# Performance work log

Measured on AMD Instinct MI355X. Metric: run time of the kernel, lower is better.

Reference implementation:

```python
import jax, jax.numpy as jnp
import numpy as np

SHAPES = ((100, 100), (50, 50), (25, 25))  # (H_l, W_l) per level
D, HEADS, HD, L, P = 256, 8, 32, 3, 4


def setup_inputs() -> dict:
    key = jax.random.key(0)
    ks = jax.random.split(key, 12)
    B = 2
    Nq = sum(h * w for h, w in SHAPES)  # 13125
    inp = {
        "query": jax.random.normal(ks[0], (B, Nq, D), jnp.float32),
        "reference_points": jax.random.uniform(ks[1], (B, Nq, L, 2), jnp.float32),
        "value0": jax.random.normal(ks[2], (B, SHAPES[0][0] * SHAPES[0][1], D), jnp.float32),
        "value1": jax.random.normal(ks[3], (B, SHAPES[1][0] * SHAPES[1][1], D), jnp.float32),
        "value2": jax.random.normal(ks[4], (B, SHAPES[2][0] * SHAPES[2][1], D), jnp.float32),
        "W_val": jax.random.normal(ks[5], (D, D), jnp.float32) * 0.05,
        "b_val": jnp.zeros((D,), jnp.float32),
        "W_off": jax.random.normal(ks[6], (D, HEADS * L * P * 2), jnp.float32) * 0.01,
        "b_off": jax.random.normal(ks[7], (HEADS * L * P * 2,), jnp.float32) * 2.0,
        "W_attn": jax.random.normal(ks[8], (D, HEADS * L * P), jnp.float32) * 0.02,
        "b_attn": jnp.zeros((HEADS * L * P,), jnp.float32),
        "W_out": jax.random.normal(ks[9], (D, D), jnp.float32) * 0.05,
        "b_out": jnp.zeros((D,), jnp.float32),
    }
    return inp


def _bilinear_sample(v, Hl, Wl, loc):
    """v: (B, heads, Hl*Wl, hd); loc: (B, Nq, heads, P, 2) normalized coords in [0,1].
    Matches torch F.grid_sample(mode='bilinear', padding_mode='zeros', align_corners=False)
    applied to grid = 2*loc - 1. Returns (B, Nq, heads, P, hd)."""
    B, heads, _, hd = v.shape
    Nq, Pn = loc.shape[1], loc.shape[3]
    # align_corners=False: pixel = ((g+1)*size - 1)/2 with g = 2*loc-1  ->  loc*size - 0.5
    x = loc[..., 0] * Wl - 0.5
    y = loc[..., 1] * Hl - 0.5
    x0 = jnp.floor(x)
    y0 = jnp.floor(y)
    wx1 = x - x0
    wy1 = y - y0
    out = jnp.zeros((B, Nq, heads, Pn, hd), v.dtype)
    for xi, wx in ((x0, 1.0 - wx1), (x0 + 1.0, wx1)):
        for yi, wy in ((y0, 1.0 - wy1), (y0 + 1.0, wy1)):
            inb = (xi >= 0) & (xi < Wl) & (yi >= 0) & (yi < Hl)
            idx = (jnp.clip(yi, 0, Hl - 1) * Wl + jnp.clip(xi, 0, Wl - 1)).astype(jnp.int32)
            idx_t = idx.transpose(0, 2, 1, 3).reshape(B, heads, Nq * Pn)  # (B,H,Nq*P)
            g = jnp.take_along_axis(v, idx_t[..., None], axis=2)  # (B,H,Nq*P,hd)
            g = g.reshape(B, heads, Nq, Pn, hd).transpose(0, 2, 1, 3, 4)
            w = (wx * wy * inb).astype(v.dtype)  # (B,Nq,heads,P)
            out = out + g * w[..., None]
    return out


def _forward(query, reference_points, values, W_val, b_val, W_off, b_off, W_attn, b_attn, W_out, b_out):
    B, Nq, _ = query.shape
    offs = (query @ W_off + b_off).reshape(B, Nq, HEADS, L, P, 2)
    attn = jax.nn.softmax((query @ W_attn + b_attn).reshape(B, Nq, HEADS, L * P), axis=-1)
    attn = attn.reshape(B, Nq, HEADS, L, P)
    out = jnp.zeros((B, Nq, HEADS, HD), query.dtype)
    for lvl, (Hl, Wl) in enumerate(SHAPES):
        # project values, split heads: (B, heads, H*W, hd)
        v = (values[lvl] @ W_val + b_val).reshape(B, Hl * Wl, HEADS, HD).transpose(0, 2, 1, 3)
        norm = jnp.array([Wl, Hl], query.dtype)
        loc = reference_points[:, :, lvl][:, :, None, None, :] + offs[:, :, :, lvl] / norm  # (B,Nq,heads,P,2)
        sampled = _bilinear_sample(v, Hl, Wl, loc)  # (B,Nq,heads,P,hd)
        out = out + jnp.einsum('bnhp,bnhpd->bnhd', attn[:, :, :, lvl], sampled)
    out = out.reshape(B, Nq, D)
    return out @ W_out + b_out  # dropout is identity at eval


def reference(query, reference_points, value0, value1, value2, W_val, b_val, W_off, b_off, W_attn, b_attn, W_out, b_out):
    return _forward(query, reference_points, (value0, value1, value2), W_val, b_val, W_off, b_off, W_attn, b_attn, W_out, b_out)
```

## Files before the change

kernel.cpp:

```cpp
#include <hip/hip_runtime.h>
#include <hip/hip_bf16.h>
#include <math.h>

#define BATCH 2
#define NQ    13125
#define MQ    26250
#define DM    256
#define NH    8
#define HDIM  32
#define NL    3
#define NP    4
#define NTOK  13125

typedef __attribute__((ext_vector_type(8))) short bf16x8;
typedef __attribute__((ext_vector_type(4))) float f32x4;
typedef __attribute__((ext_vector_type(2))) float f32x2;

__device__ __forceinline__ short f2bf(float f) {
    unsigned u = __float_as_uint(f);
    unsigned r = (u + 0x7FFFu + ((u >> 16) & 1u)) >> 16;
    return (short)r;
}
__device__ __forceinline__ float bf2f(unsigned short u) {
    return __uint_as_float((unsigned)u << 16);
}
__device__ __forceinline__ unsigned cvt_pk_bf16(float lo, float hi) {
    unsigned r;
    asm("v_cvt_pk_bf16_f32 %0, %1, %2" : "=v"(r) : "v"(lo), "v"(hi));
    return r;
}

__device__ __forceinline__ void gld_lds16(const short* g, short* l) {
    __builtin_amdgcn_global_load_lds(
        (const __attribute__((address_space(1))) unsigned int*)g,
        (__attribute__((address_space(3))) unsigned int*)l, 16, 0, 0);
}

__global__ __launch_bounds__(256) void wprep_kernel(const float* __restrict__ Wv,
                                                    const float* __restrict__ Wo,
                                                    const float* __restrict__ Wa,
                                                    const float* __restrict__ Wu,
                                                    short* __restrict__ Wt)
{
    const int bid = blockIdx.x;
    const int w  = bid >> 8;
    const int Ns[5]   = {256, 192, 96, 256, 96};
    const int Offs[5] = {0, 65536, 114688, 163840, 139264};
    const int N = Ns[w];
    const int flat = (bid & 255) * 256 + threadIdx.x;
    const int n = flat >> 8, k = flat & 255;
    if (n >= N) return;
    if (w == 4) { Wt[139264 + n * 256 + k] = 0; return; }
    const float* W = (w == 0) ? Wv : ((w == 1) ? Wo : ((w == 2) ? Wa : Wu));
    Wt[Offs[w] + n * 256 + k] = f2bf(W[k * N + n]);
}

__global__ __launch_bounds__(256) void gemm5_kernel(const float* __restrict__ query,
                                                    const float* __restrict__ v0,
                                                    const float* __restrict__ v1,
                                                    const float* __restrict__ v2,
                                                    const short* __restrict__ Wt_val,
                                                    const short* __restrict__ Wt_off,
                                                    const float* __restrict__ b_val,
                                                    const float* __restrict__ b_off,
                                                    const float* __restrict__ b_attn,
                                                    short* __restrict__ vws,
                                                    float* __restrict__ offs,
                                                    float* __restrict__ lgts)
{
    __shared__ short As[128 * 32];
    __shared__ short Bs[128 * 32];

    const int tid  = threadIdx.x;
    const int y    = blockIdx.y;
    const int m0   = blockIdx.x * 128;
    const bool isv = (y < 2);
    const short* Wt = isv ? Wt_val : Wt_off;
    const int n0 = isv ? y * 128 : (y - 2) * 128;

    const int r  = tid >> 1;
    const int h  = tid & 1;
    const int gm = m0 + r;
    const int gmc = (gm < MQ) ? gm : (MQ - 1);
    const float* Arow;
    if (isv) {
        const int b  = gmc / NTOK;
        const int rr = gmc % NTOK;
        if (rr < 10000)      Arow = v0 + (size_t)(b * 10000 + rr) * 256;
        else if (rr < 12500) Arow = v1 + (size_t)(b * 2500 + rr - 10000) * 256;
        else                 Arow = v2 + (size_t)(b * 625 + rr - 12500) * 256;
    } else {
        Arow = query + (size_t)gmc * 256;
    }
    const int pA0 = ((h * 2 + 0) ^ ((r >> 1) & 3)) << 3;
    const int pA1 = ((h * 2 + 1) ^ ((r >> 1) & 3)) << 3;
    short* lAr = As + r * 32;

    const int row0 = tid >> 2;
    const int row1 = row0 + 64;
    const int kqs  = (tid & 3) ^ ((row0 >> 1) & 3);
    const short* gB0 = Wt + (size_t)(n0 + row0) * 256 + kqs * 8;
    const short* gB1 = Wt + (size_t)(n0 + row1) * 256 + kqs * 8;
    short* lB0 = Bs + tid * 8;
    short* lB1 = Bs + (256 + tid) * 8;

    const int lane = tid & 63;
    const int wave = tid >> 6;
    const int wm   = (wave & 1) * 64;
    const int wn   = (wave >> 1) * 64;
    const int ml   = lane & 15;
    const int kq   = lane >> 4;

    f32x4 acc[4][4] = {};

    for (int k0 = 0; k0 < 256; k0 += 32) {
        gld_lds16(gB0 + k0, lB0);
        gld_lds16(gB1 + k0, lB1);

        const float4 a0 = *(const float4*)(Arow + k0 + h * 16 + 0);
        const float4 a1 = *(const float4*)(Arow + k0 + h * 16 + 4);
        const float4 a2 = *(const float4*)(Arow + k0 + h * 16 + 8);
        const float4 a3 = *(const float4*)(Arow + k0 + h * 16 + 12);
        union { bf16x8 v; unsigned u[4]; } t0, t1;
        t0.u[0] = cvt_pk_bf16(a0.x, a0.y); t0.u[1] = cvt_pk_bf16(a0.z, a0.w);
        t0.u[2] = cvt_pk_bf16(a1.x, a1.y); t0.u[3] = cvt_pk_bf16(a1.z, a1.w);
        t1.u[0] = cvt_pk_bf16(a2.x, a2.y); t1.u[1] = cvt_pk_bf16(a2.z, a2.w);
        t1.u[2] = cvt_pk_bf16(a3.x, a3.y); t1.u[3] = cvt_pk_bf16(a3.z, a3.w);
        *(bf16x8*)(lAr + pA0) = t0.v;
        *(bf16x8*)(lAr + pA1) = t1.v;

        __syncthreads();

        bf16x8 af[4], bfr[4];
#pragma unroll
        for (int ti = 0; ti < 4; ++ti) {
            const int rr = wm + ti * 16 + ml;
            af[ti] = *(const bf16x8*)&As[rr * 32 + ((kq ^ ((rr >> 1) & 3)) << 3)];
        }
#pragma unroll
        for (int tj = 0; tj < 4; ++tj) {
            const int rr = wn + tj * 16 + ml;
            bfr[tj] = *(const bf16x8*)&Bs[rr * 32 + ((kq ^ ((rr >> 1) & 3)) << 3)];
        }
#pragma unroll
        for (int ti = 0; ti < 4; ++ti)
#pragma unroll
            for (int tj = 0; tj < 4; ++tj)
                acc[ti][tj] = __builtin_amdgcn_mfma_f32_16x16x32_bf16(af[ti], bfr[tj], acc[ti][tj], 0, 0, 0);

        __syncthreads();
    }

#pragma unroll
    for (int tj = 0; tj < 4; ++tj) {
        const int gn = n0 + wn + tj * 16 + ml;
#pragma unroll
        for (int ti = 0; ti < 4; ++ti) {
#pragma unroll
            for (int rr = 0; rr < 4; ++rr) {
                const int gmo = m0 + wm + ti * 16 + kq * 4 + rr;
                if (gmo >= MQ) continue;
                const float v = acc[ti][tj][rr];
                if (isv) {
                    vws[(size_t)gmo * 256 + gn] = f2bf(v + b_val[gn]);
                } else {
                    if (gn < 192)      offs[(size_t)gmo * 192 + gn]        = v + b_off[gn];
                    else if (gn < 288) lgts[(size_t)gmo * 96 + (gn - 192)] = v + b_attn[gn - 192];
                }
            }
        }
    }
}

__device__ __forceinline__ void gemm_core128(const short* __restrict__ A,
                                             const short* __restrict__ Wt,
                                             int m0, int n0,
                                             f32x4 (&acc)[4][4],
                                             short* As, short* Bs)
{
    const int tid  = threadIdx.x;
    const int lane = tid & 63;
    const int wave = tid >> 6;
    const int wm   = (wave & 1) * 64;
    const int wn   = (wave >> 1) * 64;
    const int ml   = lane & 15;
    const int kq   = lane >> 4;

    const int row0 = tid >> 2;
    const int row1 = row0 + 64;
    const int kqs  = (tid & 3) ^ ((row0 >> 1) & 3);
    const short* gA0 = A  + (size_t)(m0 + row0) * 256 + kqs * 8;
    const short* gA1 = A  + (size_t)(m0 + row1) * 256 + kqs * 8;
    const short* gB0 = Wt + (size_t)(n0 + row0) * 256 + kqs * 8;
    const short* gB1 = Wt + (size_t)(n0 + row1) * 256 + kqs * 8;
    short* lA0 = As + tid * 8;
    short* lA1 = As + (256 + tid) * 8;
    short* lB0 = Bs + tid * 8;
    short* lB1 = Bs + (256 + tid) * 8;
    const bool a0ok = (m0 + row0) < MQ;
    const bool a1ok = (m0 + row1) < MQ;

    for (int k0 = 0; k0 < 256; k0 += 32) {
        if (a0ok) gld_lds16(gA0 + k0, lA0);
        if (a1ok) gld_lds16(gA1 + k0, lA1);
        gld_lds16(gB0 + k0, lB0);
        gld_lds16(gB1 + k0, lB1);
        __syncthreads();

        bf16x8 af[4], bfr[4];
#pragma unroll
        for (int ti = 0; ti < 4; ++ti) {
            const int r = wm + ti * 16 + ml;
            af[ti] = *(const bf16x8*)&As[r * 32 + ((kq ^ ((r >> 1) & 3)) << 3)];
        }
#pragma unroll
        for (int tj = 0; tj < 4; ++tj) {
            const int r = wn + tj * 16 + ml;
            bfr[tj] = *(const bf16x8*)&Bs[r * 32 + ((kq ^ ((r >> 1) & 3)) << 3)];
        }
#pragma unroll
        for (int ti = 0; ti < 4; ++ti)
#pragma unroll
            for (int tj = 0; tj < 4; ++tj)
                acc[ti][tj] = __builtin_amdgcn_mfma_f32_16x16x32_bf16(af[ti], bfr[tj], acc[ti][tj], 0, 0, 0);

        __syncthreads();
    }
}

__global__ __launch_bounds__(256) void ogemm_kernel(const short* __restrict__ A,
                                                    const short* __restrict__ Wt,
                                                    const float* __restrict__ bias,
                                                    float* __restrict__ C)
{
    __shared__ short As[128 * 32];
    __shared__ short Bs[128 * 32];
    const int m0 = blockIdx.y * 128;
    const int n0 = blockIdx.x * 128;

    f32x4 acc[4][4] = {};
    gemm_core128(A, Wt, m0, n0, acc, As, Bs);

    const int tid  = threadIdx.x;
    const int lane = tid & 63;
    const int wave = tid >> 6;
    const int wm   = (wave & 1) * 64;
    const int wn   = (wave >> 1) * 64;
    const int ml   = lane & 15;
    const int kq   = lane >> 4;

#pragma unroll
    for (int tj = 0; tj < 4; ++tj) {
        const int gn = n0 + wn + tj * 16 + ml;
#pragma unroll
        for (int ti = 0; ti < 4; ++ti) {
#pragma unroll
            for (int r = 0; r < 4; ++r) {
                const int gm = m0 + wm + ti * 16 + kq * 4 + r;
                if (gm >= MQ) continue;
                C[(size_t)gm * 256 + gn] = acc[ti][tj][r] + bias[gn];
            }
        }
    }
}

__device__ __forceinline__ void pk_acc(f32x2 (&acc)[4], uint4 u, float w) {
    f32x2 w2 = {w, w};
    unsigned ud[4] = {u.x, u.y, u.z, u.w};
#pragma unroll
    for (int d = 0; d < 4; ++d) {
        f32x2 v2;
        v2.x = __uint_as_float(ud[d] << 16);
        v2.y = __uint_as_float(ud[d] & 0xFFFF0000u);
        asm("v_pk_fma_f32 %0, %1, %2, %0" : "+v"(acc[d]) : "v"(v2), "v"(w2));
    }
}

__global__ __launch_bounds__(256) void sample_kernel(const short* __restrict__ vws,
                                                     const float* __restrict__ offs,
                                                     const float* __restrict__ logits,
                                                     const float* __restrict__ refp,
                                                     short* __restrict__ mid)
{
    const int q0  = blockIdx.x * 8;
    const int tid = threadIdx.x;

    __shared__ float  s_lg[8][96];
    __shared__ float  s_ref[8][6];
    __shared__ float  s_stat[8][NH][2];
    __shared__ float4 s_w[8][96];
    __shared__ int4   s_i[8][96];

    for (int idx = tid; idx < 768; idx += 256) {
        const int qq = idx / 96, s = idx % 96;
        const int q = q0 + qq;
        if (q < MQ) s_lg[qq][s] = logits[(size_t)q * 96 + s];
    }
    if (tid < 48) {
        const int qq = tid / 6, j = tid % 6;
        const int q = q0 + qq;
        if (q < MQ) s_ref[qq][j] = refp[(size_t)q * 6 + j];
    }
    __syncthreads();

    if (tid < 64) {
        const int qq = tid >> 3, h = tid & 7;
        if (q0 + qq < MQ) {
            float mx = -1e30f;
#pragma unroll
            for (int i = 0; i < 12; ++i) mx = fmaxf(mx, s_lg[qq][h * 12 + i]);
            float ssum = 0.f;
#pragma unroll
            for (int i = 0; i < 12; ++i) ssum += __expf(s_lg[qq][h * 12 + i] - mx);
            s_stat[qq][h][0] = mx;
            s_stat[qq][h][1] = 1.f / ssum;
        }
    }
    __syncthreads();

    for (int idx = tid; idx < 768; idx += 256) {
        const int qq = idx / 96, s = idx % 96;
        const int q  = q0 + qq;
        if (q >= MQ) continue;
        const int b  = q / NQ;
        const int h  = s / 12, i = s % 12;
        const int l  = i >> 2, p = i & 3;

        const int Hs[3] = {100, 50, 25};
        const int Wz[3] = {100, 50, 25};
        const int Lo[3] = {0, 10000, 12500};
        const int Wl = Wz[l], Hl = Hs[l];
        const float fW = (float)Wl, fH = (float)Hl;

        const float aw = __expf(s_lg[qq][s] - s_stat[qq][h][0]) * s_stat[qq][h][1];

        const int oi = (((h * NL) + l) * NP + p) * 2;
        const float2 offp = *(const float2*)(offs + (size_t)q * 192 + oi);
        const float rx = s_ref[qq][l * 2 + 0];
        const float ry = s_ref[qq][l * 2 + 1];

        const float x = (rx + offp.x / fW) * fW - 0.5f;
        const float y = (ry + offp.y / fH) * fH - 0.5f;
        const float x0f = floorf(x), y0f = floorf(y);
        const int   x0 = (int)x0f,  y0 = (int)y0f;
        const float wx1 = x - x0f, wy1 = y - y0f;
        const float wx0 = 1.f - wx1, wy0 = 1.f - wy1;

        const bool xin0 = (x0 >= 0) && (x0 < Wl);
        const bool xin1 = (x0 + 1 >= 0) && (x0 + 1 < Wl);
        const bool yin0 = (y0 >= 0) && (y0 < Hl);
        const bool yin1 = (y0 + 1 >= 0) && (y0 + 1 < Hl);

        const int cx0 = min(max(x0, 0), Wl - 1);
        const int cx1 = min(max(x0 + 1, 0), Wl - 1);
        const int cy0 = min(max(y0, 0), Hl - 1);
        const int cy1 = min(max(y0 + 1, 0), Hl - 1);

        const int base = b * NTOK + Lo[l];
        int4 idxv;
        idxv.x = (base + cy0 * Wl + cx0) << 8;
        idxv.y = (base + cy0 * Wl + cx1) << 8;
        idxv.z = (base + cy1 * Wl + cx0) << 8;
        idxv.w = (base + cy1 * Wl + cx1) << 8;

        float4 w;
        w.x = (xin0 && yin0) ? aw * wx0 * wy0 : 0.f;
        w.y = (xin1 && yin0) ? aw * wx1 * wy0 : 0.f;
        w.z = (xin0 && yin1) ? aw * wx0 * wy1 : 0.f;
        w.w = (xin1 && yin1) ? aw * wx1 * wy1 : 0.f;

        const int slot = i * 8 + h;
        s_w[qq][slot] = w;
        s_i[qq][slot] = idxv;
    }
    __syncthreads();

    {
        const int qq = tid >> 5;
        const int q  = q0 + qq;
        if (q < MQ) {
            const int r   = tid & 31;
            const int h   = r >> 2;
            const int chb = h * HDIM + (r & 3) * 8;

            f32x2 acc[4] = {};
#pragma unroll
            for (int s = 0; s < 12; ++s) {
                const int slot = s * 8 + h;
                const float4 w  = s_w[qq][slot];
                const int4   id = s_i[qq][slot];
                const uint4 u0 = *(const uint4*)(vws + id.x + chb);
                const uint4 u1 = *(const uint4*)(vws + id.y + chb);
                const uint4 u2 = *(const uint4*)(vws + id.z + chb);
                const uint4 u3 = *(const uint4*)(vws + id.w + chb);
                pk_acc(acc, u0, w.x);
                pk_acc(acc, u1, w.y);
                pk_acc(acc, u2, w.z);
                pk_acc(acc, u3, w.w);
            }
            uint4 o;
            o.x = cvt_pk_bf16(acc[0].x, acc[0].y);
            o.y = cvt_pk_bf16(acc[1].x, acc[1].y);
            o.z = cvt_pk_bf16(acc[2].x, acc[2].y);
            o.w = cvt_pk_bf16(acc[3].x, acc[3].y);
            *(uint4*)(mid + (size_t)q * DM + chb) = o;
        }
    }
}

extern "C" void kernel_launch(void* const* d_in, const int* in_sizes, int n_in,
                              void* d_out, int out_size, void* d_ws, size_t ws_size,
                              hipStream_t stream)
{
    const float* query  = (const float*)d_in[0];
    const float* refp   = (const float*)d_in[1];
    const float* v0     = (const float*)d_in[2];
    const float* v1     = (const float*)d_in[3];
    const float* v2     = (const float*)d_in[4];
    const float* W_val  = (const float*)d_in[5];
    const float* b_val  = (const float*)d_in[6];
    const float* W_off  = (const float*)d_in[7];
    const float* b_off  = (const float*)d_in[8];
    const float* W_attn = (const float*)d_in[9];
    const float* b_attn = (const float*)d_in[10];
    const float* W_out  = (const float*)d_in[11];
    const float* b_out  = (const float*)d_in[12];
    float* out = (float*)d_out;

    float* ws   = (float*)d_ws;
    float* offs = ws;
    float* lgts = offs + (size_t)MQ * 192;
    short* vws  = (short*)(lgts + (size_t)MQ * 96);
    short* mid  = vws + (size_t)MQ * DM;
    short* Wt   = mid + (size_t)MQ * DM;
    short* Wt_val = Wt;
    short* Wt_off = Wt + 65536;
    short* Wt_out = Wt + 163840;

    wprep_kernel<<<1280, 256, 0, stream>>>(W_val, W_off, W_attn, W_out, Wt);
    {
        dim3 grid((MQ + 127) / 128, 5);
        gemm5_kernel<<<grid, 256, 0, stream>>>(query, v0, v1, v2, Wt_val, Wt_off,
                                               b_val, b_off, b_attn, vws, offs, lgts);
    }
    sample_kernel<<<(MQ + 7) / 8, 256, 0, stream>>>(vws, offs, lgts, refp, mid);
    {
        dim3 grid(2, (MQ + 127) / 128);
        ogemm_kernel<<<grid, 256, 0, stream>>>(mid, Wt_out, b_out, out);
    }
}
```

Measured before the change: 227.2 us.

## Remap block indices across XCDs for L2 locality and prefetch gathers in sampler

The three main kernels switch to 1D grids whose block index is remapped, so each XCD (blockIdx & 7) gets a contiguous range of tiles or queries. In the sampler, batch 0 queries go to XCDs 0-3 and batch 1 to XCDs 4-7, aiming to keep each XCD's L2 holding only its own batch's value rows. The sampler's gather loop is software-pipelined so the next slot's four loads are issued before the current slot's FMAs. The attention-slot layout in shared memory is also adjusted to fit the new indexing. The hardcoded grid sizes and the remap arithmetic tie the code to this exact problem size.

```diff
diff --git a/kernel.cpp b/kernel.cpp
--- a/kernel.cpp
+++ b/kernel.cpp
@@ -68,12 +68,15 @@
                                                     float* __restrict__ offs,
                                                     float* __restrict__ lgts)
 {
+    const int e = (blockIdx.x & 7) * 129 + (blockIdx.x >> 3);
+    if (e >= 1030) return;
+    const int y  = e % 5;
+    const int m0 = (e / 5) * 128;
+
     __shared__ short As[128 * 32];
     __shared__ short Bs[128 * 32];
 
     const int tid  = threadIdx.x;
-    const int y    = blockIdx.y;
-    const int m0   = blockIdx.x * 128;
     const bool isv = (y < 2);
     const short* Wt = isv ? Wt_val : Wt_off;
     const int n0 = isv ? y * 128 : (y - 2) * 128;
@@ -233,10 +236,13 @@
                                                     const float* __restrict__ bias,
                                                     float* __restrict__ C)
 {
+    const int e = (blockIdx.x & 7) * 52 + (blockIdx.x >> 3);
+    if (e >= 412) return;
+    const int m0 = (e >> 1) * 128;
+    const int n0 = (e & 1) * 128;
+
     __shared__ short As[128 * 32];
     __shared__ short Bs[128 * 32];
-    const int m0 = blockIdx.y * 128;
-    const int n0 = blockIdx.x * 128;
 
     f32x4 acc[4][4] = {};
     gemm_core128(A, Wt, m0, n0, acc, As, Bs);
@@ -282,7 +288,12 @@
                                                      const float* __restrict__ refp,
                                                      short* __restrict__ mid)
 {
-    const int q0  = blockIdx.x * 8;
+    const int bid = blockIdx.x;
+    const int xcd = bid & 7, pos = bid >> 3;
+    int g;
+    if (xcd < 4) { g = pos * 4 + xcd; }
+    else         { g = 1644 + pos * 4 + (xcd - 4); if (g >= 3282) return; }
+    const int q0  = g * 8;
     const int tid = threadIdx.x;
 
     __shared__ float  s_lg[8][96];
@@ -319,11 +330,11 @@
     __syncthreads();
 
     for (int idx = tid; idx < 768; idx += 256) {
-        const int qq = idx / 96, s = idx % 96;
+        const int qq = idx / 96, slot = idx % 96;
         const int q  = q0 + qq;
         if (q >= MQ) continue;
         const int b  = q / NQ;
-        const int h  = s / 12, i = s % 12;
+        const int h  = slot & 7, i = slot >> 3;
         const int l  = i >> 2, p = i & 3;
 
         const int Hs[3] = {100, 50, 25};
@@ -332,7 +343,7 @@
         const int Wl = Wz[l], Hl = Hs[l];
         const float fW = (float)Wl, fH = (float)Hl;
 
-        const float aw = __expf(s_lg[qq][s] - s_stat[qq][h][0]) * s_stat[qq][h][1];
+        const float aw = __expf(s_lg[qq][h * 12 + i] - s_stat[qq][h][0]) * s_stat[qq][h][1];
 
         const int oi = (((h * NL) + l) * NP + p) * 2;
         const float2 offp = *(const float2*)(offs + (size_t)q * 192 + oi);
@@ -369,7 +380,6 @@
         w.z = (xin0 && yin1) ? aw * wx0 * wy1 : 0.f;
         w.w = (xin1 && yin1) ? aw * wx1 * wy1 : 0.f;
 
-        const int slot = i * 8 + h;
         s_w[qq][slot] = w;
         s_i[qq][slot] = idxv;
     }
@@ -382,21 +392,33 @@
             const int r   = tid & 31;
             const int h   = r >> 2;
             const int chb = h * HDIM + (r & 3) * 8;
+            const short* base = vws + chb;
+
+            float4 w_ = s_w[qq][h];
+            int4  id_ = s_i[qq][h];
+            uint4 a_ = *(const uint4*)(base + id_.x);
+            uint4 b_ = *(const uint4*)(base + id_.y);
+            uint4 c_ = *(const uint4*)(base + id_.z);
+            uint4 d_ = *(const uint4*)(base + id_.w);
 
             f32x2 acc[4] = {};
 #pragma unroll
             for (int s = 0; s < 12; ++s) {
-                const int slot = s * 8 + h;
-                const float4 w  = s_w[qq][slot];
-                const int4   id = s_i[qq][slot];
-                const uint4 u0 = *(const uint4*)(vws + id.x + chb);
-                const uint4 u1 = *(const uint4*)(vws + id.y + chb);
-                const uint4 u2 = *(const uint4*)(vws + id.z + chb);
-                const uint4 u3 = *(const uint4*)(vws + id.w + chb);
-                pk_acc(acc, u0, w.x);
-                pk_acc(acc, u1, w.y);
-                pk_acc(acc, u2, w.z);
-                pk_acc(acc, u3, w.w);
+                const float4 w = w_;
+                const uint4 ua = a_, ub = b_, uc = c_, ud = d_;
+                if (s < 11) {
+                    const int slot = (s + 1) * 8 + h;
+                    w_  = s_w[qq][slot];
+                    id_ = s_i[qq][slot];
+                    a_ = *(const uint4*)(base + id_.x);
+                    b_ = *(const uint4*)(base + id_.y);
+                    c_ = *(const uint4*)(base + id_.z);
+                    d_ = *(const uint4*)(base + id_.w);
+                }
+                pk_acc(acc, ua, w.x);
+                pk_acc(acc, ub, w.y);
+                pk_acc(acc, uc, w.z);
+                pk_acc(acc, ud, w.w);
             }
             uint4 o;
             o.x = cvt_pk_bf16(acc[0].x, acc[0].y);
@@ -438,14 +460,8 @@
     short* Wt_out = Wt + 163840;
 
     wprep_kernel<<<1280, 256, 0, stream>>>(W_val, W_off, W_attn, W_out, Wt);
-    {
-        dim3 grid((MQ + 127) / 128, 5);
-        gemm5_kernel<<<grid, 256, 0, stream>>>(query, v0, v1, v2, Wt_val, Wt_off,
-                                               b_val, b_off, b_attn, vws, offs, lgts);
-    }
-    sample_kernel<<<(MQ + 7) / 8, 256, 0, stream>>>(vws, offs, lgts, refp, mid);
-    {
-        dim3 grid(2, (MQ + 127) / 128);
-        ogemm_kernel<<<grid, 256, 0, stream>>>(mid, Wt_out, b_out, out);
-    }
-}
+    gemm5_kernel<<<1032, 256, 0, stream>>>(query, v0, v1, v2, Wt_val, Wt_off,
+                                           b_val, b_off, b_attn, vws, offs, lgts);
+    sample_kernel<<<3288, 256, 0, stream>>>(vws, offs, lgts, refp, mid);
+    ogemm_kernel<<<416, 256, 0, stream>>>(mid, Wt_out, b_out, out);
+}
```

Result: no change. 227.6 us (+0.2%).
